# Kernel tuning notes

Hardware: AMD Instinct MI355X
Metric: run time of the kernel (lower is better)

Reference implementation:

```python
import jax, jax.numpy as jnp
import numpy as np

B, IDF, CDF, IH, IW, SL = 32, 768, 768, 32, 32, 128

def setup_inputs() -> dict:
    key = jax.random.key(0)
    k1, k2, k3, k4 = jax.random.split(key, 4)
    inp = jax.random.normal(k1, (B, IDF, IH, IW), dtype=jnp.float32)
    ctx = jax.random.normal(k2, (B, CDF, SL), dtype=jnp.float32)
    mask = jax.random.randint(k3, (B, SL), 0, 2, dtype=jnp.int32)
    # 1x1 conv with no bias == matmul weight [idf, cdf]
    w_conv = jax.random.normal(k4, (IDF, CDF), dtype=jnp.float32) * 0.02
    return {"input": inp, "context": ctx, "mask": mask, "w_conv": w_conv}

def reference(input, context, mask, w_conv):
    b, idf, ih, iw = input.shape
    queryL = ih * iw
    sourceL = context.shape[2]
    # target: b x idf x queryL
    target = input.reshape(b, idf, queryL)
    # 1x1 conv projection of context: b x idf x sourceL
    sourceT = jnp.einsum('oc,bcs->bos', w_conv, context)
    # attention logits: b x queryL x sourceL (targetT @ sourceT)
    attn = jnp.einsum('biq,bis->bqs', target, sourceT)
    attn = attn + mask[:, None, :].astype(attn.dtype) * (-10000.0)
    attn = jax.nn.softmax(attn, axis=-1)  # softmax over sourceL
    # weighted context: sourceT @ attn^T -> b x idf x queryL
    weightedContext = jnp.einsum('bis,bqs->biq', sourceT, attn).reshape(b, idf, ih, iw)
    attn_out = jnp.transpose(attn, (0, 2, 1)).reshape(b, sourceL, ih, iw)
    return weightedContext, attn_out
```

## Files before the change

### kernel.cpp

```cpp
#include <hip/hip_runtime.h>

#define NB  32
#define IDF 768
#define SLN 128
#define QLN 1024
#define NT2 12

typedef _Float16 v8hf __attribute__((ext_vector_type(8)));
typedef _Float16 v4hf __attribute__((ext_vector_type(4)));
typedef float    v4f  __attribute__((ext_vector_type(4)));

#define MFMAH __builtin_amdgcn_mfma_f32_16x16x32_f16

__device__ __forceinline__ void gload16(const void* g, void* l) {
  __builtin_amdgcn_global_load_lds(
      (const __attribute__((address_space(1))) void*)g,
      (__attribute__((address_space(3))) void*)l, 16, 0, 0);
}

__device__ __forceinline__ void lbar() {
  asm volatile("s_waitcnt lgkmcnt(0)" ::: "memory");
  __builtin_amdgcn_sched_barrier(0);
  __builtin_amdgcn_s_barrier();
  __builtin_amdgcn_sched_barrier(0);
}

__global__ __launch_bounds__(256) void prep_k(const float* __restrict__ W,
                                              const float* __restrict__ ctx,
                                              _Float16* __restrict__ Wf,
                                              _Float16* __restrict__ cTf) {
  const int bid = blockIdx.x, t = threadIdx.x;
  __shared__ float tl[64][133];
  if (bid < 576) {
    int idx = bid * 1024 + t * 4;
    float4 v = *(const float4*)(W + idx);
    v4hf h;
    h[0] = (_Float16)v.x;
    h[1] = (_Float16)v.y;
    h[2] = (_Float16)v.z;
    h[3] = (_Float16)v.w;
    *(v4hf*)(Wf + idx) = h;
    return;
  }
  const int cid = bid - 576;
  const int b = cid / 12, c0 = (cid % 12) * 64;
#pragma unroll
  for (int j = 0; j < 8; ++j) {
    int u = j * 256 + t;
    int c = u >> 5, s4 = (u & 31) * 4;
    *(float4*)&tl[c][s4] =
        *(const float4*)(ctx + ((size_t)b * IDF + c0 + c) * SLN + s4);
  }
  __syncthreads();
#pragma unroll
  for (int j = 0; j < 8; ++j) {
    int u = j * 256 + t;
    int s = u >> 4, c4 = (u & 15) * 4;
    v4hf h;
#pragma unroll
    for (int e = 0; e < 4; ++e) h[e] = (_Float16)tl[c4 + e][s];
    *(v4hf*)(cTf + ((size_t)b * SLN + s) * IDF + c0 + c4) = h;
  }
}

__global__ __launch_bounds__(256) void proj_k(const _Float16* __restrict__ cTf,
                                              const _Float16* __restrict__ Wf,
                                              _Float16* __restrict__ STf,
                                              _Float16* __restrict__ Shvf) {
  const int b = blockIdx.y, o0 = blockIdx.x * 32;
  const int t = threadIdx.x, w = t >> 6, lane = t & 63;
  const int lr = lane & 15, lg = lane >> 4;
  const int ws = w >> 1, wq = w & 1;
  __shared__ _Float16 AL[128][72];

  v4f acc[4];
#pragma unroll
  for (int fr = 0; fr < 4; ++fr) acc[fr] = (v4f){0.f, 0.f, 0.f, 0.f};

  const int ra = t >> 1;
  const int cb = (t & 1) * 4;
  const _Float16* pA = cTf + ((size_t)b * SLN + ra) * IDF + cb * 8;
  const size_t wOff = (size_t)(o0 + wq * 16 + lr) * IDF + lg * 8;

  uint4 aS0, aS1, aS2, aS3, bS0, bS1, bS2, bS3;
  v8hf wc0, wc1, wn0, wn1;
  aS0 = *(const uint4*)(pA);
  aS1 = *(const uint4*)(pA + 8);
  aS2 = *(const uint4*)(pA + 16);
  aS3 = *(const uint4*)(pA + 24);
  bS0 = *(const uint4*)(pA + 64);
  bS1 = *(const uint4*)(pA + 72);
  bS2 = *(const uint4*)(pA + 80);
  bS3 = *(const uint4*)(pA + 88);
  wc0 = *(const v8hf*)(Wf + wOff);
  wc1 = *(const v8hf*)(Wf + wOff + 32);

#define PROJ_BODY(S0, S1, S2, S3, IT)                                          \
  {                                                                            \
    lbar();                                                                    \
    *(uint4*)&AL[ra][(cb + 0) * 8] = S0;                                       \
    *(uint4*)&AL[ra][(cb + 1) * 8] = S1;                                       \
    *(uint4*)&AL[ra][(cb + 2) * 8] = S2;                                       \
    *(uint4*)&AL[ra][(cb + 3) * 8] = S3;                                       \
    if ((IT) + 2 < NT2) {                                                      \
      S0 = *(const uint4*)(pA + ((IT) + 2) * 64);                              \
      S1 = *(const uint4*)(pA + ((IT) + 2) * 64 + 8);                          \
      S2 = *(const uint4*)(pA + ((IT) + 2) * 64 + 16);                         \
      S3 = *(const uint4*)(pA + ((IT) + 2) * 64 + 24);                         \
    }                                                                          \
    if ((IT) + 1 < NT2) {                                                      \
      wn0 = *(const v8hf*)(Wf + wOff + ((IT) + 1) * 64);                       \
      wn1 = *(const v8hf*)(Wf + wOff + ((IT) + 1) * 64 + 32);                  \
    }                                                                          \
    lbar();                                                                    \
    _Pragma("unroll") for (int fr = 0; fr < 4; ++fr) {                         \
      const int r = ws * 64 + fr * 16 + lr;                                    \
      v8hf ah0 = *(const v8hf*)&AL[r][lg * 8];                                 \
      acc[fr] = MFMAH(ah0, wc0, acc[fr], 0, 0, 0);                             \
      v8hf ah1 = *(const v8hf*)&AL[r][32 + lg * 8];                            \
      acc[fr] = MFMAH(ah1, wc1, acc[fr], 0, 0, 0);                             \
    }                                                                          \
    wc0 = wn0;                                                                 \
    wc1 = wn1;                                                                 \
  }

  for (int it2 = 0; it2 < NT2 / 2; ++it2) {
    const int itE = it2 * 2;
    PROJ_BODY(aS0, aS1, aS2, aS3, itE);
    PROJ_BODY(bS0, bS1, bS2, bS3, itE + 1);
  }
#undef PROJ_BODY

  const int o = o0 + wq * 16 + lr;
#pragma unroll
  for (int fr = 0; fr < 4; ++fr) {
    v4hf hp;
#pragma unroll
    for (int r = 0; r < 4; ++r) {
      int s = ws * 64 + fr * 16 + lg * 4 + r;
      _Float16 h = (_Float16)acc[fr][r];
      STf[((size_t)b * SLN + s) * IDF + o] = h;
      hp[r] = h;
    }
    *(v4hf*)(Shvf + ((size_t)b * IDF + o) * SLN + ws * 64 + fr * 16 + lg * 4) =
        hp;
  }
}

__global__ __launch_bounds__(256, 4) void qkpv_k(const float* __restrict__ input,
                                                 const _Float16* __restrict__ STf,
                                                 const _Float16* __restrict__ Shvf,
                                                 const int* __restrict__ mask,
                                                 float* __restrict__ wc,
                                                 float* __restrict__ attn_out) {
  const int bid = blockIdx.x;
  const int nid = (bid & 7) * 64 + (bid >> 3);
  const int b = nid >> 4, q0 = (nid & 15) * 64;
  const int t = threadIdx.x, w = t >> 6, lane = t & 63;
  const int lr = lane & 15, lg = lane >> 4;
  const int wqp = w & 1, sh2 = w >> 1;

  __shared__ __align__(16) char lds[34304];
  float* const msk  = (float*)(lds + 32768);
  float* const redm = (float*)(lds + 33280);
  float* const reds = (float*)(lds + 33792);
  char* const PLb = lds;

  if (t < SLN) msk[t] = -10000.0f * (float)mask[b * SLN + t];

  v4f acc[4][2];
#pragma unroll
  for (int fr = 0; fr < 4; ++fr)
#pragma unroll
    for (int j = 0; j < 2; ++j) acc[fr][j] = (v4f){0.f, 0.f, 0.f, 0.f};

  const int rA = (lane >> 3);
  const int cpA = lane & 7;
  const _Float16* gA[4];
#pragma unroll
  for (int g = 0; g < 4; ++g) {
    const int row = w * 32 + g * 8 + rA;
    const int c = cpA ^ (row & 7);
    gA[g] = STf + ((size_t)b * SLN + row) * IDF + c * 8;
  }
  const int dA = w * 4096;

  const float* gB = input + (size_t)b * IDF * QLN + q0 + wqp * 32 + lr;

#pragma unroll
  for (int g = 0; g < 4; ++g) gload16(gA[g], lds + dA + g * 1024);
  v8hf aH[2][2], bH[2][2];
  float tmpB[2][2][8];
#pragma unroll
  for (int kk = 0; kk < 2; ++kk)
#pragma unroll
    for (int j = 0; j < 2; ++j)
#pragma unroll
      for (int e = 0; e < 8; ++e)
        tmpB[kk][j][e] = gB[(size_t)(kk * 32 + lg * 8 + e) * QLN + j * 16];
#pragma unroll
  for (int kk = 0; kk < 2; ++kk)
#pragma unroll
    for (int j = 0; j < 2; ++j)
#pragma unroll
      for (int e = 0; e < 8; ++e) aH[kk][j][e] = (_Float16)tmpB[kk][j][e];
#pragma unroll
  for (int g = 0; g < 4; ++g) gload16(gA[g] + 64, lds + 16384 + dA + g * 1024);

#define QK_WIN(CUROFF, BC, BN, IT, VMC)                                        \
  {                                                                            \
    asm volatile("s_waitcnt vmcnt(" #VMC ")" ::: "memory");                    \
    __builtin_amdgcn_sched_barrier(0);                                         \
    __builtin_amdgcn_s_barrier();                                              \
    __builtin_amdgcn_sched_barrier(0);                                         \
    if ((IT) + 1 < NT2) {                                                      \
      _Pragma("unroll") for (int kk = 0; kk < 2; ++kk)                         \
          _Pragma("unroll") for (int j = 0; j < 2; ++j)                        \
          _Pragma("unroll") for (int e = 0; e < 8; ++e)                        \
          tmpB[kk][j][e] =                                                     \
              gB[(size_t)(((IT) + 1) * 64 + kk * 32 + lg * 8 + e) * QLN +      \
                 j * 16];                                                      \
    }                                                                          \
    __builtin_amdgcn_sched_barrier(0);                                         \
    const char* Ab = lds + (CUROFF);                                           \
    __builtin_amdgcn_s_setprio(1);                                             \
    _Pragma("unroll") for (int fr = 0; fr < 4; ++fr) {                         \
      const int r = sh2 * 64 + fr * 16 + lr;                                   \
      _Pragma("unroll") for (int kk = 0; kk < 2; ++kk) {                       \
        const int cc = (kk * 4 + lg) ^ (r & 7);                                \
        v8hf ah = *(const v8hf*)(Ab + r * 128 + cc * 16);                      \
        _Pragma("unroll") for (int j = 0; j < 2; ++j) {                        \
          acc[fr][j] = MFMAH(ah, BC[kk][j], acc[fr][j], 0, 0, 0);              \
        }                                                                      \
      }                                                                        \
    }                                                                          \
    __builtin_amdgcn_s_setprio(0);                                             \
    __builtin_amdgcn_sched_barrier(0);                                         \
    if ((IT) + 1 < NT2) {                                                      \
      _Pragma("unroll") for (int kk = 0; kk < 2; ++kk)                         \
          _Pragma("unroll") for (int j = 0; j < 2; ++j)                        \
          _Pragma("unroll") for (int e = 0; e < 8; ++e)                        \
          BN[kk][j][e] = (_Float16)tmpB[kk][j][e];                             \
    }                                                                          \
    asm volatile("s_waitcnt lgkmcnt(0)" ::: "memory");                         \
    __builtin_amdgcn_s_barrier();                                              \
    if ((IT) + 2 < NT2) {                                                      \
      _Pragma("unroll") for (int g = 0; g < 4; ++g)                            \
          gload16(gA[g] + (size_t)((IT) + 2) * 64,                             \
                  lds + (CUROFF) + dA + g * 1024);                             \
    }                                                                          \
  }

  for (int it2 = 0; it2 < 5; ++it2) {
    const int itE = it2 * 2;
    QK_WIN(0, aH, bH, itE, 4);
    QK_WIN(16384, bH, aH, itE + 1, 4);
  }
  QK_WIN(0, aH, bH, 10, 4);
  QK_WIN(16384, bH, aH, 11, 0);
#undef QK_WIN

  float mx[2], sum[2];
#pragma unroll
  for (int j = 0; j < 2; ++j) {
    mx[j] = -3.0e38f;
#pragma unroll
    for (int fr = 0; fr < 4; ++fr)
#pragma unroll
      for (int r = 0; r < 4; ++r) {
        acc[fr][j][r] += msk[sh2 * 64 + fr * 16 + lg * 4 + r];
        mx[j] = fmaxf(mx[j], acc[fr][j][r]);
      }
    mx[j] = fmaxf(mx[j], __shfl_xor(mx[j], 16));
    mx[j] = fmaxf(mx[j], __shfl_xor(mx[j], 32));
    if (lg == 0) redm[sh2 * 64 + wqp * 32 + j * 16 + lr] = mx[j];
  }
  __syncthreads();
#pragma unroll
  for (int j = 0; j < 2; ++j) {
    const int qh = wqp * 32 + j * 16 + lr;
    mx[j] = fmaxf(redm[qh], redm[64 + qh]);
    sum[j] = 0.f;
#pragma unroll
    for (int fr = 0; fr < 4; ++fr)
#pragma unroll
      for (int r = 0; r < 4; ++r) {
        float e = __expf(acc[fr][j][r] - mx[j]);
        acc[fr][j][r] = e;
        sum[j] += e;
      }
    sum[j] += __shfl_xor(sum[j], 16);
    sum[j] += __shfl_xor(sum[j], 32);
    if (lg == 0) reds[sh2 * 64 + wqp * 32 + j * 16 + lr] = sum[j];
  }
  __syncthreads();
#pragma unroll
  for (int j = 0; j < 2; ++j) {
    const int qh = wqp * 32 + j * 16 + lr;
    const float inv = 1.0f / (reds[qh] + reds[64 + qh]);
    const int q = q0 + qh;
#pragma unroll
    for (int fr = 0; fr < 4; ++fr) {
      v4hf hp;
#pragma unroll
      for (int r = 0; r < 4; ++r) {
        float p = acc[fr][j][r] * inv;
        attn_out[((size_t)b * SLN + sh2 * 64 + fr * 16 + lg * 4 + r) * QLN + q] =
            p;
        hp[r] = (_Float16)p;
      }
      const int g = (sh2 * 8 + fr * 2 + (lg >> 1)) ^ lr;
      *(v4hf*)(PLb + qh * 256 + g * 16 + (lg & 1) * 8) = hp;
    }
  }
  __syncthreads();

  const int qfp = (w & 1) * 2;
  const int islab = (w >> 1) * 384;
  v8hf pa0v[4], pa1v[4];
#pragma unroll
  for (int kt = 0; kt < 4; ++kt) {
    const int g0 = (kt * 4 + lg) ^ lr;
    pa0v[kt] = *(const v8hf*)(PLb + (qfp * 16 + lr) * 256 + g0 * 16);
    pa1v[kt] = *(const v8hf*)(PLb + ((qfp + 1) * 16 + lr) * 256 + g0 * 16);
  }
  const _Float16* pShv = Shvf + ((size_t)b * IDF + islab + lr) * SLN + lg * 8;
  float* pWc = wc + ((size_t)b * IDF + islab + lr) * QLN + q0;
#pragma unroll 2
  for (int ifr = 0; ifr < 24; ++ifr) {
    v4f a0 = (v4f){0.f, 0.f, 0.f, 0.f};
    v4f a1 = (v4f){0.f, 0.f, 0.f, 0.f};
#pragma unroll
    for (int kt = 0; kt < 4; ++kt) {
      v8hf bb = *(const v8hf*)(pShv + (size_t)(ifr * 16) * SLN + kt * 32);
      a0 = MFMAH(pa0v[kt], bb, a0, 0, 0, 0);
      a1 = MFMAH(pa1v[kt], bb, a1, 0, 0, 0);
    }
    *(float4*)(pWc + (size_t)(ifr * 16) * QLN + qfp * 16 + lg * 4) =
        make_float4(a0[0], a0[1], a0[2], a0[3]);
    *(float4*)(pWc + (size_t)(ifr * 16) * QLN + (qfp + 1) * 16 + lg * 4) =
        make_float4(a1[0], a1[1], a1[2], a1[3]);
  }
}

extern "C" void kernel_launch(void* const* d_in, const int* in_sizes, int n_in,
                              void* d_out, int out_size, void* d_ws, size_t ws_size,
                              hipStream_t stream) {
  const float* input   = (const float*)d_in[0];
  const float* context = (const float*)d_in[1];
  const int*   mask    = (const int*)d_in[2];
  const float* w_conv  = (const float*)d_in[3];

  float* out      = (float*)d_out;
  float* wc       = out;
  float* attn_out = out + (size_t)NB * IDF * QLN;

  const size_t SE = (size_t)NB * SLN * IDF;
  _Float16* wsb = (_Float16*)d_ws;
  _Float16* STf  = wsb;
  _Float16* Shvf = STf + SE;
  _Float16* scr  = (_Float16*)wc;
  _Float16* cTf  = scr;
  _Float16* Wf   = cTf + SE;

  prep_k<<<960, 256, 0, stream>>>(w_conv, context, Wf, cTf);
  proj_k<<<dim3(24, NB), 256, 0, stream>>>(cTf, Wf, STf, Shvf);
  qkpv_k<<<512, 256, 0, stream>>>(input, STf, Shvf, mask, wc, attn_out);
}
```

Baseline: 79.32 us.

## Give each wave a full source row range to drop cross-wave softmax reductions

The QK^T stage changes its wave tiling. Before, each wave covered 32 queries by 64 source positions. Now each wave covers 16 queries across all 128 source positions, so every softmax row lives inside one wave. That removes the LDS max/sum reduction buffers and two block-wide barriers. In exchange, each B fragment (input converted to fp16) now feeds 8 MFMAs instead of 2 per A load, while A-tile LDS reads double per wave, which changes LDS traffic and register use.

```diff
diff --git a/kernel.cpp b/kernel.cpp
--- a/kernel.cpp
+++ b/kernel.cpp
@@ -158,21 +158,16 @@
   const int b = nid >> 4, q0 = (nid & 15) * 64;
   const int t = threadIdx.x, w = t >> 6, lane = t & 63;
   const int lr = lane & 15, lg = lane >> 4;
-  const int wqp = w & 1, sh2 = w >> 1;
-
-  __shared__ __align__(16) char lds[34304];
-  float* const msk  = (float*)(lds + 32768);
-  float* const redm = (float*)(lds + 33280);
-  float* const reds = (float*)(lds + 33792);
+
+  __shared__ __align__(16) char lds[33280];
+  float* const msk = (float*)(lds + 32768);
   char* const PLb = lds;
 
   if (t < SLN) msk[t] = -10000.0f * (float)mask[b * SLN + t];
 
-  v4f acc[4][2];
-#pragma unroll
-  for (int fr = 0; fr < 4; ++fr)
-#pragma unroll
-    for (int j = 0; j < 2; ++j) acc[fr][j] = (v4f){0.f, 0.f, 0.f, 0.f};
+  v4f acc[8];
+#pragma unroll
+  for (int fr = 0; fr < 8; ++fr) acc[fr] = (v4f){0.f, 0.f, 0.f, 0.f};
 
   const int rA = (lane >> 3);
   const int cpA = lane & 7;
@@ -185,25 +180,21 @@
   }
   const int dA = w * 4096;
 
-  const float* gB = input + (size_t)b * IDF * QLN + q0 + wqp * 32 + lr;
+  const float* gB = input + (size_t)b * IDF * QLN + q0 + w * 16 + lr;
 
 #pragma unroll
   for (int g = 0; g < 4; ++g) gload16(gA[g], lds + dA + g * 1024);
-  v8hf aH[2][2], bH[2][2];
-  float tmpB[2][2][8];
+  v8hf aH[2], bH[2];
+  float tmpB[2][8];
 #pragma unroll
   for (int kk = 0; kk < 2; ++kk)
 #pragma unroll
-    for (int j = 0; j < 2; ++j)
-#pragma unroll
-      for (int e = 0; e < 8; ++e)
-        tmpB[kk][j][e] = gB[(size_t)(kk * 32 + lg * 8 + e) * QLN + j * 16];
+    for (int e = 0; e < 8; ++e)
+      tmpB[kk][e] = gB[(size_t)(kk * 32 + lg * 8 + e) * QLN];
 #pragma unroll
   for (int kk = 0; kk < 2; ++kk)
 #pragma unroll
-    for (int j = 0; j < 2; ++j)
-#pragma unroll
-      for (int e = 0; e < 8; ++e) aH[kk][j][e] = (_Float16)tmpB[kk][j][e];
+    for (int e = 0; e < 8; ++e) aH[kk][e] = (_Float16)tmpB[kk][e];
 #pragma unroll
   for (int g = 0; g < 4; ++g) gload16(gA[g] + 64, lds + 16384 + dA + g * 1024);
 
@@ -215,32 +206,27 @@
     __builtin_amdgcn_sched_barrier(0);                                         \
     if ((IT) + 1 < NT2) {                                                      \
       _Pragma("unroll") for (int kk = 0; kk < 2; ++kk)                         \
-          _Pragma("unroll") for (int j = 0; j < 2; ++j)                        \
           _Pragma("unroll") for (int e = 0; e < 8; ++e)                        \
-          tmpB[kk][j][e] =                                                     \
-              gB[(size_t)(((IT) + 1) * 64 + kk * 32 + lg * 8 + e) * QLN +      \
-                 j * 16];                                                      \
+          tmpB[kk][e] =                                                        \
+              gB[(size_t)(((IT) + 1) * 64 + kk * 32 + lg * 8 + e) * QLN];      \
     }                                                                          \
     __builtin_amdgcn_sched_barrier(0);                                         \
     const char* Ab = lds + (CUROFF);                                           \
     __builtin_amdgcn_s_setprio(1);                                             \
-    _Pragma("unroll") for (int fr = 0; fr < 4; ++fr) {                         \
-      const int r = sh2 * 64 + fr * 16 + lr;                                   \
+    _Pragma("unroll") for (int fr = 0; fr < 8; ++fr) {                         \
+      const int r = fr * 16 + lr;                                              \
       _Pragma("unroll") for (int kk = 0; kk < 2; ++kk) {                       \
         const int cc = (kk * 4 + lg) ^ (r & 7);                                \
         v8hf ah = *(const v8hf*)(Ab + r * 128 + cc * 16);                      \
-        _Pragma("unroll") for (int j = 0; j < 2; ++j) {                        \
-          acc[fr][j] = MFMAH(ah, BC[kk][j], acc[fr][j], 0, 0, 0);              \
-        }                                                                      \
+        acc[fr] = MFMAH(ah, BC[kk], acc[fr], 0, 0, 0);                         \
       }                                                                        \
     }                                                                          \
     __builtin_amdgcn_s_setprio(0);                                             \
     __builtin_amdgcn_sched_barrier(0);                                         \
     if ((IT) + 1 < NT2) {                                                      \
       _Pragma("unroll") for (int kk = 0; kk < 2; ++kk)                         \
-          _Pragma("unroll") for (int j = 0; j < 2; ++j)                        \
           _Pragma("unroll") for (int e = 0; e < 8; ++e)                        \
-          BN[kk][j][e] = (_Float16)tmpB[kk][j][e];                             \
+          BN[kk][e] = (_Float16)tmpB[kk][e];                                   \
     }                                                                          \
     asm volatile("s_waitcnt lgkmcnt(0)" ::: "memory");                         \
     __builtin_amdgcn_s_barrier();                                              \
@@ -260,58 +246,41 @@
   QK_WIN(16384, bH, aH, 11, 0);
 #undef QK_WIN
 
-  float mx[2], sum[2];
-#pragma unroll
-  for (int j = 0; j < 2; ++j) {
-    mx[j] = -3.0e38f;
-#pragma unroll
-    for (int fr = 0; fr < 4; ++fr)
-#pragma unroll
-      for (int r = 0; r < 4; ++r) {
-        acc[fr][j][r] += msk[sh2 * 64 + fr * 16 + lg * 4 + r];
-        mx[j] = fmaxf(mx[j], acc[fr][j][r]);
-      }
-    mx[j] = fmaxf(mx[j], __shfl_xor(mx[j], 16));
-    mx[j] = fmaxf(mx[j], __shfl_xor(mx[j], 32));
-    if (lg == 0) redm[sh2 * 64 + wqp * 32 + j * 16 + lr] = mx[j];
-  }
-  __syncthreads();
-#pragma unroll
-  for (int j = 0; j < 2; ++j) {
-    const int qh = wqp * 32 + j * 16 + lr;
-    mx[j] = fmaxf(redm[qh], redm[64 + qh]);
-    sum[j] = 0.f;
-#pragma unroll
-    for (int fr = 0; fr < 4; ++fr)
-#pragma unroll
-      for (int r = 0; r < 4; ++r) {
-        float e = __expf(acc[fr][j][r] - mx[j]);
-        acc[fr][j][r] = e;
-        sum[j] += e;
-      }
-    sum[j] += __shfl_xor(sum[j], 16);
-    sum[j] += __shfl_xor(sum[j], 32);
-    if (lg == 0) reds[sh2 * 64 + wqp * 32 + j * 16 + lr] = sum[j];
-  }
-  __syncthreads();
-#pragma unroll
-  for (int j = 0; j < 2; ++j) {
-    const int qh = wqp * 32 + j * 16 + lr;
-    const float inv = 1.0f / (reds[qh] + reds[64 + qh]);
-    const int q = q0 + qh;
-#pragma unroll
-    for (int fr = 0; fr < 4; ++fr) {
-      v4hf hp;
-#pragma unroll
-      for (int r = 0; r < 4; ++r) {
-        float p = acc[fr][j][r] * inv;
-        attn_out[((size_t)b * SLN + sh2 * 64 + fr * 16 + lg * 4 + r) * QLN + q] =
-            p;
-        hp[r] = (_Float16)p;
-      }
-      const int g = (sh2 * 8 + fr * 2 + (lg >> 1)) ^ lr;
-      *(v4hf*)(PLb + qh * 256 + g * 16 + (lg & 1) * 8) = hp;
-    }
+  const int qh = w * 16 + lr;
+  float mx = -3.0e38f;
+#pragma unroll
+  for (int fr = 0; fr < 8; ++fr)
+#pragma unroll
+    for (int r = 0; r < 4; ++r) {
+      acc[fr][r] += msk[fr * 16 + lg * 4 + r];
+      mx = fmaxf(mx, acc[fr][r]);
+    }
+  mx = fmaxf(mx, __shfl_xor(mx, 16));
+  mx = fmaxf(mx, __shfl_xor(mx, 32));
+  float sum = 0.f;
+#pragma unroll
+  for (int fr = 0; fr < 8; ++fr)
+#pragma unroll
+    for (int r = 0; r < 4; ++r) {
+      float e = __expf(acc[fr][r] - mx);
+      acc[fr][r] = e;
+      sum += e;
+    }
+  sum += __shfl_xor(sum, 16);
+  sum += __shfl_xor(sum, 32);
+  const float inv = 1.0f / sum;
+  const int q = q0 + qh;
+#pragma unroll
+  for (int fr = 0; fr < 8; ++fr) {
+    v4hf hp;
+#pragma unroll
+    for (int r = 0; r < 4; ++r) {
+      float p = acc[fr][r] * inv;
+      attn_out[((size_t)b * SLN + fr * 16 + lg * 4 + r) * QLN + q] = p;
+      hp[r] = (_Float16)p;
+    }
+    const int g = (fr * 2 + (lg >> 1)) ^ lr;
+    *(v4hf*)(PLb + qh * 256 + g * 16 + (lg & 1) * 8) = hp;
   }
   __syncthreads();
 
```

After: 78.07 us. Within noise of the previous version (-1.6%).
